# Kernel optimization log

Measured on AMD Instinct MI355X. Metric: run time of the kernel, lower is better.

The kernel has to match this reference:

```python
import jax, jax.numpy as jnp
import numpy as np

N, E, D_IN, D_H, D_OUT, L = 100000, 1000000, 128, 64, 40, 7
MSG_EPS = 1e-7   # GENConv message epsilon
BN_EPS = 1e-5    # torch BatchNorm1d eps
T = 1.0          # softmax temperature (learn_t=False)


def _segment_softmax(logits, seg, n):
    # numerically stable softmax over edges grouped by destination node
    m = jax.ops.segment_max(logits, seg, num_segments=n)
    e = jnp.exp(logits - m[seg])
    s = jax.ops.segment_sum(e, seg, num_segments=n)
    return e / (s[seg] + 1e-16)


def _gen_conv(h, src, dst, W, b):
    # GENConv, aggr='softmax_sg', mlp_layers=1, msg_norm=False
    msg = jax.nn.relu(h[src]) + MSG_EPS                 # [E, D_H]
    w = jax.lax.stop_gradient(_segment_softmax(msg * T, dst, N))
    agg = jax.ops.segment_sum(w * msg, dst, num_segments=N)  # [N, D_H]
    return (h + agg) @ W + b


def _batch_norm(h, gamma, beta):
    mu = jnp.mean(h, axis=0)
    var = jnp.mean(jnp.square(h - mu), axis=0)  # biased var (training mode)
    return gamma * (h - mu) * jax.lax.rsqrt(var + BN_EPS) + beta


def setup_inputs() -> dict:
    key = jax.random.key(0)
    ks = jax.random.split(key, 6)
    x = jax.random.normal(ks[0], (N, D_IN), dtype=jnp.float32)
    edge_index = jax.random.randint(ks[1], (2, E), 0, N, dtype=jnp.int64)
    W_enc = jax.random.normal(ks[2], (D_IN, D_H), dtype=jnp.float32) / np.float32(np.sqrt(D_IN))
    b_enc = jnp.zeros((D_H,), jnp.float32)
    Wg = jax.random.normal(ks[3], (L, D_H, D_H), dtype=jnp.float32) / np.float32(np.sqrt(D_H))
    bg = jnp.zeros((L, D_H), jnp.float32)
    gamma = jnp.ones((L, D_H), jnp.float32)
    beta = jnp.zeros((L, D_H), jnp.float32)
    W_pred = jax.random.normal(ks[4], (D_H, D_OUT), dtype=jnp.float32) / np.float32(np.sqrt(D_H))
    b_pred = jnp.zeros((D_OUT,), jnp.float32)
    return {"x": x, "edge_index": edge_index, "W_enc": W_enc, "b_enc": b_enc,
            "Wg": Wg, "bg": bg, "gamma": gamma, "beta": beta,
            "W_pred": W_pred, "b_pred": b_pred}


def reference(x, edge_index, W_enc, b_enc, Wg, bg, gamma, beta, W_pred, b_pred):
    src, dst = edge_index[0], edge_index[1]
    h = x @ W_enc + b_enc                               # node encoder
    h = _gen_conv(h, src, dst, Wg[0], bg[0])            # first conv (res+)
    for layer in range(1, L):                            # BN->ReLU->Conv->Res
        h2 = jax.nn.relu(_batch_norm(h, gamma[layer - 1], beta[layer - 1]))
        h = _gen_conv(h2, src, dst, Wg[layer], bg[layer]) + h
    h = jax.nn.relu(_batch_norm(h, gamma[L - 1], beta[L - 1]))
    logits = h @ W_pred + b_pred
    return jax.nn.log_softmax(logits, axis=-1)
```

## Files before the change

### kernel.cpp

```cpp
#include <hip/hip_runtime.h>
#include <math.h>

#define NN 100000
#define NE 1000000
#define DH 64
#define DIN 128
#define DOUT 40
#define NL 7
#define SCAN_B 1024
#define NBLK ((NN + SCAN_B - 1) / SCAN_B)
#define NGRP (NN / 16)
#define LBLK ((NGRP + 3) / 4)
#define COLB_CAP (NE + 16 * NN + 64)
#define QS 16.0f
#define IQS 0.0625f

typedef _Float16 v8h __attribute__((ext_vector_type(8)));
typedef float v4f __attribute__((ext_vector_type(4)));

__global__ __launch_bounds__(256) void k_count2(const int* __restrict__ dst,
                                                int* __restrict__ cnt,
                                                int* __restrict__ pi) {
  int i = blockIdx.x * 256 + threadIdx.x;
  if (i < NE) pi[i] = atomicAdd(&cnt[dst[i]], 1);
}

__global__ __launch_bounds__(SCAN_B) void k_scan1(const int* __restrict__ cnt,
                                                  int* __restrict__ rp16,
                                                  int* __restrict__ bsum) {
  __shared__ int buf[SCAN_B];
  int i = blockIdx.x * SCAN_B + threadIdx.x;
  int v = (i < NN) ? ((cnt[i] + 15) & ~15) : 0;
  buf[threadIdx.x] = v;
  __syncthreads();
  for (int off = 1; off < SCAN_B; off <<= 1) {
    int t = (threadIdx.x >= off) ? buf[threadIdx.x - off] : 0;
    __syncthreads();
    buf[threadIdx.x] += t;
    __syncthreads();
  }
  if (i < NN) rp16[i] = buf[threadIdx.x] - v;
  if (threadIdx.x == SCAN_B - 1) bsum[blockIdx.x] = buf[SCAN_B - 1];
}

__global__ __launch_bounds__(128) void k_scan2(int* __restrict__ bsum) {
  __shared__ int buf[128];
  int v = (threadIdx.x < NBLK) ? bsum[threadIdx.x] : 0;
  buf[threadIdx.x] = v;
  __syncthreads();
  for (int off = 1; off < 128; off <<= 1) {
    int t = (threadIdx.x >= off) ? buf[threadIdx.x - off] : 0;
    __syncthreads();
    buf[threadIdx.x] += t;
    __syncthreads();
  }
  if (threadIdx.x < NBLK) bsum[threadIdx.x] = buf[threadIdx.x] - v;
}

__global__ __launch_bounds__(SCAN_B) void k_scan3(int* __restrict__ rp16,
                                                  const int* __restrict__ bsum) {
  int i = blockIdx.x * SCAN_B + threadIdx.x;
  if (i < NN) rp16[i] += bsum[blockIdx.x];
}

__global__ __launch_bounds__(256) void k_place(const int* __restrict__ src,
                                               const int* __restrict__ dst,
                                               const int* __restrict__ rp16,
                                               const int* __restrict__ pi,
                                               int* __restrict__ colb) {
  int i = blockIdx.x * 256 + threadIdx.x;
  if (i < NE) colb[rp16[dst[i]] + pi[i]] = src[i] * DH;
}

__global__ __launch_bounds__(256) void k_enc_mfma(const float* __restrict__ x,
                                                  const float* __restrict__ W,
                                                  const float* __restrict__ b,
                                                  float* __restrict__ h) {
  __shared__ _Float16 Atile[4][2048];
  const int tid = threadIdx.x;
  const int w = tid >> 6, lane = tid & 63;
  const int gid = blockIdx.x * 4 + w;
  if (gid >= NGRP) return;
  const int row = lane & 15, hi = lane >> 4;

  v8h bf[4][4];
#pragma unroll
  for (int kt = 0; kt < 4; ++kt)
#pragma unroll
    for (int ct = 0; ct < 4; ++ct)
#pragma unroll
      for (int j = 0; j < 8; ++j)
        bf[kt][ct][j] = (_Float16)W[(kt * 32 + hi * 8 + j) * DH + ct * 16 + row];

  const int base = gid * 16;
  _Float16* At = &Atile[w][0];
#pragma unroll 4
  for (int i = 0; i < 16; ++i) {
    float v0 = x[(size_t)(base + i) * DIN + lane];
    float v1 = x[(size_t)(base + i) * DIN + 64 + lane];
    int swi = (i & 7) << 4;
    At[(i * 256 + ((lane * 2) ^ swi)) >> 1] = (_Float16)v0;
    At[(i * 256 + 128 + ((lane * 2) ^ swi)) >> 1] = (_Float16)v1;
  }
  const int sw = (row & 7) << 4;
  v8h a[4];
#pragma unroll
  for (int kt = 0; kt < 4; ++kt) {
    int off = (kt & 1) * 64 + hi * 16;
    a[kt] = *(const v8h*)&At[(row * 256 + (kt >> 1) * 128 + (off ^ sw)) >> 1];
  }
  v4f c0 = {0, 0, 0, 0}, c1 = {0, 0, 0, 0}, c2 = {0, 0, 0, 0}, c3 = {0, 0, 0, 0};
#pragma unroll
  for (int kt = 0; kt < 4; ++kt) {
    c0 = __builtin_amdgcn_mfma_f32_16x16x32_f16(a[kt], bf[kt][0], c0, 0, 0, 0);
    c1 = __builtin_amdgcn_mfma_f32_16x16x32_f16(a[kt], bf[kt][1], c1, 0, 0, 0);
    c2 = __builtin_amdgcn_mfma_f32_16x16x32_f16(a[kt], bf[kt][2], c2, 0, 0, 0);
    c3 = __builtin_amdgcn_mfma_f32_16x16x32_f16(a[kt], bf[kt][3], c3, 0, 0, 0);
  }
  float b0 = b[row], b1 = b[16 + row], b2 = b[32 + row], b3 = b[48 + row];
#pragma unroll
  for (int reg = 0; reg < 4; ++reg) {
    size_t o = (size_t)(base + hi * 4 + reg) * DH;
    h[o + row] = c0[reg] + b0;
    h[o + 16 + row] = c1[reg] + b1;
    h[o + 32 + row] = c2[reg] + b2;
    h[o + 48 + row] = c3[reg] + b3;
  }
}

__global__ __launch_bounds__(256) void k_msg(const float* __restrict__ h,
                                             const float* __restrict__ stats_in,
                                             const float* __restrict__ gamma,
                                             const float* __restrict__ beta,
                                             unsigned char* __restrict__ msg) {
  int lane = threadIdx.x & 63;
  float scale = 1.f, shift = 0.f;
  if (stats_in) {
    float mu = stats_in[lane] * (1.0f / NN);
    float var = stats_in[64 + lane] * (1.0f / NN) - mu * mu;
    scale = gamma[lane] * rsqrtf(var + 1e-5f);
    shift = beta[lane] - mu * scale;
  }
  int wid = (blockIdx.x * blockDim.x + threadIdx.x) >> 6;
  int nw = (gridDim.x * blockDim.x) >> 6;
  for (int n = wid; n < NN; n += nw) {
    float r = h[n * DH + lane];
    float v = fmaxf(fmaf(r, scale, shift), 0.f) + 1e-7f;
    msg[n * DH + lane] = (unsigned char)fminf(v * QS + 0.5f, 255.f);
  }
}

__global__ __launch_bounds__(256, 8) void k_agg(const unsigned char* __restrict__ msg,
                                                const int* __restrict__ rp16,
                                                const int* __restrict__ cnt,
                                                const int* __restrict__ colb,
                                                _Float16* __restrict__ agg) {
  const int lane = threadIdx.x & 63;
  const int n = (blockIdx.x * 256 + threadIdx.x) >> 6;
  const int beg = rp16[n];
  const int deg = cnt[n];
  const unsigned char* mb = msg + lane;
  float s = 0.f, t = 0.f;
  for (int j = 0; j < deg; j += 16) {
    int cc[16];
#pragma unroll
    for (int k = 0; k < 16; ++k) cc[k] = colb[beg + j + k];
    float vv[16];
#pragma unroll
    for (int k = 0; k < 16; ++k) vv[k] = (float)mb[cc[k]] * IQS;
    int rem = deg - j;
#pragma unroll
    for (int k = 0; k < 16; ++k) {
      float e = (k < rem) ? __expf(vv[k]) : 0.f;
      s += e;
      t = fmaf(e, vv[k], t);
    }
  }
  agg[(size_t)n * DH + lane] = (_Float16)(t / (s + 1e-16f));
}

__global__ __launch_bounds__(256) void k_mfma(
    const float* __restrict__ h_pre, const _Float16* __restrict__ agg,
    const float* __restrict__ stats_in,
    const float* __restrict__ gamma, const float* __restrict__ beta,
    const float* __restrict__ W, const float* __restrict__ b, int add_res,
    float* __restrict__ hout, float* __restrict__ partial) {
  __shared__ _Float16 Atile[4][1024];
  const int tid = threadIdx.x;
  const int w = tid >> 6, lane = tid & 63;
  const int gid = blockIdx.x * 4 + w;
  const int row = lane & 15, hi = lane >> 4;

  float ss0 = 0, ss1 = 0, ss2 = 0, ss3 = 0;
  float qq0 = 0, qq1 = 0, qq2 = 0, qq3 = 0;

  if (gid < NGRP) {
    float scale = 1.f, shift = 0.f;
    if (stats_in) {
      float mu = stats_in[lane] * (1.0f / NN);
      float var = stats_in[64 + lane] * (1.0f / NN) - mu * mu;
      scale = gamma[lane] * rsqrtf(var + 1e-5f);
      shift = beta[lane] - mu * scale;
    }
    v8h bf[2][4];
#pragma unroll
    for (int kt = 0; kt < 2; ++kt)
#pragma unroll
      for (int ct = 0; ct < 4; ++ct)
#pragma unroll
        for (int j = 0; j < 8; ++j)
          bf[kt][ct][j] = (_Float16)W[(kt * 32 + hi * 8 + j) * DH + ct * 16 + row];

    const int base = gid * 16;
    const float* hl = h_pre + lane;
    const _Float16* agl = agg + lane;
    _Float16* At = &Atile[w][0];

    float rawv[16], agv[16];
#pragma unroll
    for (int i = 0; i < 16; ++i) {
      size_t o = (size_t)(base + i) * DH;
      rawv[i] = hl[o];
      agv[i] = (float)agl[o];
    }
    float res[4][4];
    if (add_res) {
#pragma unroll
      for (int reg = 0; reg < 4; ++reg) {
        size_t o = (size_t)(base + hi * 4 + reg) * DH;
        res[reg][0] = h_pre[o + row];
        res[reg][1] = h_pre[o + 16 + row];
        res[reg][2] = h_pre[o + 32 + row];
        res[reg][3] = h_pre[o + 48 + row];
      }
    }
#pragma unroll
    for (int i = 0; i < 16; ++i) {
      float v = stats_in ? fmaxf(fmaf(rawv[i], scale, shift), 0.f) : rawv[i];
      v += agv[i];
      At[(i * 128 + ((lane * 2) ^ ((i & 7) << 4))) >> 1] = (_Float16)v;
    }
    const int sw = (row & 7) << 4;
    v8h a0 = *(const v8h*)&At[((row * 128) + ((hi * 16) ^ sw)) >> 1];
    v8h a1 = *(const v8h*)&At[((row * 128) + ((64 + hi * 16) ^ sw)) >> 1];
    v4f c0 = {0, 0, 0, 0}, c1 = {0, 0, 0, 0}, c2 = {0, 0, 0, 0}, c3 = {0, 0, 0, 0};
    c0 = __builtin_amdgcn_mfma_f32_16x16x32_f16(a0, bf[0][0], c0, 0, 0, 0);
    c0 = __builtin_amdgcn_mfma_f32_16x16x32_f16(a1, bf[1][0], c0, 0, 0, 0);
    c1 = __builtin_amdgcn_mfma_f32_16x16x32_f16(a0, bf[0][1], c1, 0, 0, 0);
    c1 = __builtin_amdgcn_mfma_f32_16x16x32_f16(a1, bf[1][1], c1, 0, 0, 0);
    c2 = __builtin_amdgcn_mfma_f32_16x16x32_f16(a0, bf[0][2], c2, 0, 0, 0);
    c2 = __builtin_amdgcn_mfma_f32_16x16x32_f16(a1, bf[1][2], c2, 0, 0, 0);
    c3 = __builtin_amdgcn_mfma_f32_16x16x32_f16(a0, bf[0][3], c3, 0, 0, 0);
    c3 = __builtin_amdgcn_mfma_f32_16x16x32_f16(a1, bf[1][3], c3, 0, 0, 0);

    float b0 = b[row], b1 = b[16 + row], b2 = b[32 + row], b3 = b[48 + row];
#pragma unroll
    for (int reg = 0; reg < 4; ++reg) {
      size_t o = (size_t)(base + hi * 4 + reg) * DH;
      float a0v = c0[reg] + b0;
      float a1v = c1[reg] + b1;
      float a2v = c2[reg] + b2;
      float a3v = c3[reg] + b3;
      if (add_res) {
        a0v += res[reg][0];
        a1v += res[reg][1];
        a2v += res[reg][2];
        a3v += res[reg][3];
      }
      hout[o + row] = a0v;
      hout[o + 16 + row] = a1v;
      hout[o + 32 + row] = a2v;
      hout[o + 48 + row] = a3v;
      ss0 += a0v; qq0 = fmaf(a0v, a0v, qq0);
      ss1 += a1v; qq1 = fmaf(a1v, a1v, qq1);
      ss2 += a2v; qq2 = fmaf(a2v, a2v, qq2);
      ss3 += a3v; qq3 = fmaf(a3v, a3v, qq3);
    }
  }

#pragma unroll
  for (int off = 16; off <= 32; off <<= 1) {
    ss0 += __shfl_xor(ss0, off, 64); ss1 += __shfl_xor(ss1, off, 64);
    ss2 += __shfl_xor(ss2, off, 64); ss3 += __shfl_xor(ss3, off, 64);
    qq0 += __shfl_xor(qq0, off, 64); qq1 += __shfl_xor(qq1, off, 64);
    qq2 += __shfl_xor(qq2, off, 64); qq3 += __shfl_xor(qq3, off, 64);
  }
  __syncthreads();
  float* Sr = (float*)&Atile[0][0];
  if (lane < 16) {
    Sr[w * 128 + lane] = ss0;       Sr[w * 128 + 16 + lane] = ss1;
    Sr[w * 128 + 32 + lane] = ss2;  Sr[w * 128 + 48 + lane] = ss3;
    Sr[w * 128 + 64 + lane] = qq0;  Sr[w * 128 + 80 + lane] = qq1;
    Sr[w * 128 + 96 + lane] = qq2;  Sr[w * 128 + 112 + lane] = qq3;
  }
  __syncthreads();
  if (tid < 128) {
    float vsum = Sr[tid] + Sr[128 + tid] + Sr[256 + tid] + Sr[384 + tid];
    partial[(size_t)blockIdx.x * 128 + tid] = vsum;
  }
}

__global__ __launch_bounds__(256) void k_red(const float* __restrict__ partial,
                                             float* __restrict__ stats) {
  const int f = blockIdx.x;
  float acc = 0.f;
  for (int i = threadIdx.x; i < LBLK; i += 256)
    acc += partial[(size_t)i * 128 + f];
  __shared__ float buf[256];
  buf[threadIdx.x] = acc;
  __syncthreads();
  for (int off = 128; off >= 1; off >>= 1) {
    if (threadIdx.x < off) buf[threadIdx.x] += buf[threadIdx.x + off];
    __syncthreads();
  }
  if (threadIdx.x == 0) stats[f] = buf[0];
}

__global__ __launch_bounds__(256) void k_pred_mfma(
    const float* __restrict__ h_pre, const float* __restrict__ stats_in,
    const float* __restrict__ gamma, const float* __restrict__ beta,
    const float* __restrict__ Wp, const float* __restrict__ bp,
    float* __restrict__ out) {
  __shared__ _Float16 Atile[4][1024];
  const int tid = threadIdx.x;
  const int w = tid >> 6, lane = tid & 63;
  const int gid = blockIdx.x * 4 + w;
  if (gid >= NGRP) return;
  const int row = lane & 15, hi = lane >> 4;

  float mu = stats_in[lane] * (1.0f / NN);
  float var = stats_in[64 + lane] * (1.0f / NN) - mu * mu;
  float scale = gamma[lane] * rsqrtf(var + 1e-5f);
  float shift = beta[lane] - mu * scale;

  v8h bf[2][3];
#pragma unroll
  for (int kt = 0; kt < 2; ++kt)
#pragma unroll
    for (int ct = 0; ct < 3; ++ct) {
      int n = ct * 16 + row;
#pragma unroll
      for (int j = 0; j < 8; ++j)
        bf[kt][ct][j] =
            (n < DOUT) ? (_Float16)Wp[(kt * 32 + hi * 8 + j) * DOUT + n]
                       : (_Float16)0.f;
    }

  const int base = gid * 16;
  const float* hl = h_pre + lane;
  _Float16* At = &Atile[w][0];
#pragma unroll 4
  for (int i = 0; i < 16; ++i) {
    float raw = hl[(size_t)(base + i) * DH];
    float v = fmaxf(fmaf(raw, scale, shift), 0.f);
    At[(i * 128 + ((lane * 2) ^ ((i & 7) << 4))) >> 1] = (_Float16)v;
  }
  const int sw = (row & 7) << 4;
  v8h a0 = *(const v8h*)&At[((row * 128) + ((hi * 16) ^ sw)) >> 1];
  v8h a1 = *(const v8h*)&At[((row * 128) + ((64 + hi * 16) ^ sw)) >> 1];
  v4f c0 = {0, 0, 0, 0}, c1 = {0, 0, 0, 0}, c2 = {0, 0, 0, 0};
  c0 = __builtin_amdgcn_mfma_f32_16x16x32_f16(a0, bf[0][0], c0, 0, 0, 0);
  c0 = __builtin_amdgcn_mfma_f32_16x16x32_f16(a1, bf[1][0], c0, 0, 0, 0);
  c1 = __builtin_amdgcn_mfma_f32_16x16x32_f16(a0, bf[0][1], c1, 0, 0, 0);
  c1 = __builtin_amdgcn_mfma_f32_16x16x32_f16(a1, bf[1][1], c1, 0, 0, 0);
  c2 = __builtin_amdgcn_mfma_f32_16x16x32_f16(a0, bf[0][2], c2, 0, 0, 0);
  c2 = __builtin_amdgcn_mfma_f32_16x16x32_f16(a1, bf[1][2], c2, 0, 0, 0);

  float bp0 = bp[row], bp1 = bp[16 + row];
  float bp2 = (32 + row < DOUT) ? bp[32 + row] : 0.f;
  bool v2 = (32 + row) < DOUT;
#pragma unroll
  for (int reg = 0; reg < 4; ++reg) {
    float l0 = c0[reg] + bp0;
    float l1 = c1[reg] + bp1;
    float l2 = v2 ? (c2[reg] + bp2) : -INFINITY;
    float xm = fmaxf(fmaxf(l0, l1), l2);
#pragma unroll
    for (int off = 1; off <= 8; off <<= 1) xm = fmaxf(xm, __shfl_xor(xm, off, 64));
    float e = __expf(l0 - xm) + __expf(l1 - xm) + (v2 ? __expf(l2 - xm) : 0.f);
#pragma unroll
    for (int off = 1; off <= 8; off <<= 1) e += __shfl_xor(e, off, 64);
    float ls = xm + __logf(e);
    size_t o = (size_t)(base + hi * 4 + reg) * DOUT;
    out[o + row] = l0 - ls;
    out[o + 16 + row] = l1 - ls;
    if (v2) out[o + 32 + row] = l2 - ls;
  }
}

extern "C" void kernel_launch(void* const* d_in, const int* in_sizes, int n_in,
                              void* d_out, int out_size, void* d_ws, size_t ws_size,
                              hipStream_t stream) {
  const float* x      = (const float*)d_in[0];
  const int*   ei     = (const int*)d_in[1];
  const float* W_enc  = (const float*)d_in[2];
  const float* b_enc  = (const float*)d_in[3];
  const float* Wg     = (const float*)d_in[4];
  const float* bg     = (const float*)d_in[5];
  const float* gamma  = (const float*)d_in[6];
  const float* beta   = (const float*)d_in[7];
  const float* W_pred = (const float*)d_in[8];
  const float* b_pred = (const float*)d_in[9];
  float* out = (float*)d_out;

  const int* src = ei;
  const int* dst = ei + NE;

  char* p = (char*)d_ws;
  auto alloc = [&](size_t bytes) -> void* {
    void* r = (void*)p;
    p += (bytes + 255) & ~(size_t)255;
    return r;
  };
  float*         hA      = (float*)alloc((size_t)NN * DH * 4);
  float*         hB      = (float*)alloc((size_t)NN * DH * 4);
  unsigned char* msg     = (unsigned char*)alloc((size_t)NN * DH);
  _Float16*      agg     = (_Float16*)alloc((size_t)NN * DH * 2);
  int*           rp16    = (int*)alloc((size_t)(NN + 1) * 4);
  int*           pi      = (int*)alloc((size_t)NE * 4);
  int*           cnt     = (int*)alloc((size_t)NN * 4);
  int*           colb    = (int*)alloc((size_t)COLB_CAP * 4);
  int*           bsum    = (int*)alloc((size_t)NBLK * 4);
  float*         stats   = (float*)alloc((size_t)NL * 128 * 4);
  float*         partial = (float*)alloc((size_t)LBLK * 128 * 4);

  hipMemsetAsync(cnt, 0, (size_t)NN * 4, stream);
  hipMemsetAsync(colb, 0, (size_t)COLB_CAP * 4, stream);

  k_count2<<<(NE + 255) / 256, 256, 0, stream>>>(dst, cnt, pi);
  k_scan1<<<NBLK, SCAN_B, 0, stream>>>(cnt, rp16, bsum);
  k_scan2<<<1, 128, 0, stream>>>(bsum);
  k_scan3<<<NBLK, SCAN_B, 0, stream>>>(rp16, bsum);
  k_place<<<(NE + 255) / 256, 256, 0, stream>>>(src, dst, rp16, pi, colb);

  k_enc_mfma<<<LBLK, 256, 0, stream>>>(x, W_enc, b_enc, hA);

  const int MSG_BLOCKS = 1024;
  const int AGG_BLOCKS = NN * 64 / 256;

  k_msg<<<MSG_BLOCKS, 256, 0, stream>>>(hA, nullptr, nullptr, nullptr, msg);
  k_agg<<<AGG_BLOCKS, 256, 0, stream>>>(msg, rp16, cnt, colb, agg);
  k_mfma<<<LBLK, 256, 0, stream>>>(
      hA, agg, nullptr, nullptr, nullptr, Wg, bg, 0, hB, partial);
  k_red<<<128, 256, 0, stream>>>(partial, stats);

  float* h = hB;
  float* hn = hA;
  for (int l = 1; l < NL; ++l) {
    const float* st = stats + (size_t)(l - 1) * 128;
    const float* g  = gamma + (size_t)(l - 1) * DH;
    const float* be = beta + (size_t)(l - 1) * DH;
    k_msg<<<MSG_BLOCKS, 256, 0, stream>>>(h, st, g, be, msg);
    k_agg<<<AGG_BLOCKS, 256, 0, stream>>>(msg, rp16, cnt, colb, agg);
    k_mfma<<<LBLK, 256, 0, stream>>>(
        h, agg, st, g, be,
        Wg + (size_t)l * DH * DH, bg + (size_t)l * DH, 1,
        hn, partial);
    k_red<<<128, 256, 0, stream>>>(partial, stats + (size_t)l * 128);
    float* tmp = h; h = hn; hn = tmp;
  }

  k_pred_mfma<<<LBLK, 256, 0, stream>>>(
      h, stats + (size_t)(NL - 1) * 128,
      gamma + (size_t)(NL - 1) * DH, beta + (size_t)(NL - 1) * DH,
      W_pred, b_pred, out);
}
```

Measured before the change: 554.0 us.

## Pad CSR to 8 with a zero-message sentinel row and split count atomics

Degree padding in the CSR drops from 16 to 8. Padded slots now point at a zeroed sentinel message row (offset DH), so the aggregation loop runs without per-element masking and afterwards subtracts the padding's exp(0) contributions from the denominator. Edge counting spreads atomics over four sub-counters per node to reduce contention, which needs extra per-node sub-offsets in the scan and placement kernels. Row begin and degree are made wave-uniform with readfirstlane. The cost is extra scan work and memory, and more exp calls on padded slots.

Measured after the change: 517.5 us. -6.6%, faster.

```diff
diff --git a/kernel.cpp b/kernel.cpp
--- a/kernel.cpp
+++ b/kernel.cpp
@@ -11,27 +11,37 @@
 #define NBLK ((NN + SCAN_B - 1) / SCAN_B)
 #define NGRP (NN / 16)
 #define LBLK ((NGRP + 3) / 4)
-#define COLB_CAP (NE + 16 * NN + 64)
+#define COLB_CAP (NE + 8 * NN + 64)
 #define QS 16.0f
 #define IQS 0.0625f
 
 typedef _Float16 v8h __attribute__((ext_vector_type(8)));
 typedef float v4f __attribute__((ext_vector_type(4)));
 
-__global__ __launch_bounds__(256) void k_count2(const int* __restrict__ dst,
-                                                int* __restrict__ cnt,
+__global__ __launch_bounds__(256) void k_count4(const int* __restrict__ dst,
+                                                int* __restrict__ cnt4,
                                                 int* __restrict__ pi) {
   int i = blockIdx.x * 256 + threadIdx.x;
-  if (i < NE) pi[i] = atomicAdd(&cnt[dst[i]], 1);
-}
-
-__global__ __launch_bounds__(SCAN_B) void k_scan1(const int* __restrict__ cnt,
-                                                  int* __restrict__ rp16,
+  if (i < NE) pi[i] = atomicAdd(&cnt4[(size_t)(i & 3) * NN + dst[i]], 1);
+}
+
+__global__ __launch_bounds__(SCAN_B) void k_scan1(const int* __restrict__ cnt4,
+                                                  int* __restrict__ cnt,
+                                                  int* __restrict__ rp8,
+                                                  int* __restrict__ rp8s,
                                                   int* __restrict__ bsum) {
   __shared__ int buf[SCAN_B];
   int i = blockIdx.x * SCAN_B + threadIdx.x;
-  int v = (i < NN) ? ((cnt[i] + 15) & ~15) : 0;
-  buf[threadIdx.x] = v;
+  int c0 = 0, c1 = 0, c2 = 0, c3 = 0;
+  if (i < NN) {
+    c0 = cnt4[i];
+    c1 = cnt4[(size_t)NN + i];
+    c2 = cnt4[(size_t)2 * NN + i];
+    c3 = cnt4[(size_t)3 * NN + i];
+  }
+  int tot = c0 + c1 + c2 + c3;
+  int t8 = (tot + 7) & ~7;
+  buf[threadIdx.x] = t8;
   __syncthreads();
   for (int off = 1; off < SCAN_B; off <<= 1) {
     int t = (threadIdx.x >= off) ? buf[threadIdx.x - off] : 0;
@@ -39,7 +49,15 @@
     buf[threadIdx.x] += t;
     __syncthreads();
   }
-  if (i < NN) rp16[i] = buf[threadIdx.x] - v;
+  if (i < NN) {
+    int excl = buf[threadIdx.x] - t8;
+    cnt[i] = tot;
+    rp8[i] = excl;
+    rp8s[4 * i] = excl;
+    rp8s[4 * i + 1] = excl + c0;
+    rp8s[4 * i + 2] = excl + c0 + c1;
+    rp8s[4 * i + 3] = excl + c0 + c1 + c2;
+  }
   if (threadIdx.x == SCAN_B - 1) bsum[blockIdx.x] = buf[SCAN_B - 1];
 }
 
@@ -57,19 +75,28 @@
   if (threadIdx.x < NBLK) bsum[threadIdx.x] = buf[threadIdx.x] - v;
 }
 
-__global__ __launch_bounds__(SCAN_B) void k_scan3(int* __restrict__ rp16,
+__global__ __launch_bounds__(SCAN_B) void k_scan3(int* __restrict__ rp8,
+                                                  int* __restrict__ rp8s,
                                                   const int* __restrict__ bsum) {
   int i = blockIdx.x * SCAN_B + threadIdx.x;
-  if (i < NN) rp16[i] += bsum[blockIdx.x];
+  if (i < NN) {
+    int b = bsum[blockIdx.x];
+    rp8[i] += b;
+    rp8s[4 * i] += b;
+    rp8s[4 * i + 1] += b;
+    rp8s[4 * i + 2] += b;
+    rp8s[4 * i + 3] += b;
+  }
 }
 
 __global__ __launch_bounds__(256) void k_place(const int* __restrict__ src,
                                                const int* __restrict__ dst,
-                                               const int* __restrict__ rp16,
+                                               const int* __restrict__ rp8s,
                                                const int* __restrict__ pi,
                                                int* __restrict__ colb) {
   int i = blockIdx.x * 256 + threadIdx.x;
-  if (i < NE) colb[rp16[dst[i]] + pi[i]] = src[i] * DH;
+  if (i < NE)
+    colb[rp8s[4 * dst[i] + (i & 3)] + pi[i]] = src[i] * DH + DH;
 }
 
 __global__ __launch_bounds__(256) void k_enc_mfma(const float* __restrict__ x,
@@ -146,36 +173,37 @@
   for (int n = wid; n < NN; n += nw) {
     float r = h[n * DH + lane];
     float v = fmaxf(fmaf(r, scale, shift), 0.f) + 1e-7f;
-    msg[n * DH + lane] = (unsigned char)fminf(v * QS + 0.5f, 255.f);
+    msg[DH + n * DH + lane] = (unsigned char)fminf(v * QS + 0.5f, 255.f);
   }
 }
 
 __global__ __launch_bounds__(256, 8) void k_agg(const unsigned char* __restrict__ msg,
-                                                const int* __restrict__ rp16,
+                                                const int* __restrict__ rp8,
                                                 const int* __restrict__ cnt,
                                                 const int* __restrict__ colb,
                                                 _Float16* __restrict__ agg) {
   const int lane = threadIdx.x & 63;
   const int n = (blockIdx.x * 256 + threadIdx.x) >> 6;
-  const int beg = rp16[n];
-  const int deg = cnt[n];
+  const int beg = __builtin_amdgcn_readfirstlane(rp8[n]);
+  const int deg = __builtin_amdgcn_readfirstlane(cnt[n]);
+  const int pdeg = (deg + 7) & ~7;
   const unsigned char* mb = msg + lane;
   float s = 0.f, t = 0.f;
-  for (int j = 0; j < deg; j += 16) {
-    int cc[16];
-#pragma unroll
-    for (int k = 0; k < 16; ++k) cc[k] = colb[beg + j + k];
-    float vv[16];
-#pragma unroll
-    for (int k = 0; k < 16; ++k) vv[k] = (float)mb[cc[k]] * IQS;
-    int rem = deg - j;
-#pragma unroll
-    for (int k = 0; k < 16; ++k) {
-      float e = (k < rem) ? __expf(vv[k]) : 0.f;
+  for (int j = 0; j < pdeg; j += 8) {
+    int cc[8];
+#pragma unroll
+    for (int k = 0; k < 8; ++k) cc[k] = colb[beg + j + k];
+    float vv[8];
+#pragma unroll
+    for (int k = 0; k < 8; ++k) vv[k] = (float)mb[cc[k]] * IQS;
+#pragma unroll
+    for (int k = 0; k < 8; ++k) {
+      float e = __expf(vv[k]);
       s += e;
       t = fmaf(e, vv[k], t);
     }
   }
+  s -= (float)(pdeg - deg);
   agg[(size_t)n * DH + lane] = (_Float16)(t / (s + 1e-16f));
 }
 
@@ -414,24 +442,27 @@
   };
   float*         hA      = (float*)alloc((size_t)NN * DH * 4);
   float*         hB      = (float*)alloc((size_t)NN * DH * 4);
-  unsigned char* msg     = (unsigned char*)alloc((size_t)NN * DH);
+  unsigned char* msg     = (unsigned char*)alloc((size_t)(NN + 1) * DH);
   _Float16*      agg     = (_Float16*)alloc((size_t)NN * DH * 2);
-  int*           rp16    = (int*)alloc((size_t)(NN + 1) * 4);
+  int*           rp8     = (int*)alloc((size_t)NN * 4);
+  int*           rp8s    = (int*)alloc((size_t)NN * 4 * 4);
   int*           pi      = (int*)alloc((size_t)NE * 4);
   int*           cnt     = (int*)alloc((size_t)NN * 4);
+  int*           cnt4    = (int*)alloc((size_t)NN * 4 * 4);
   int*           colb    = (int*)alloc((size_t)COLB_CAP * 4);
   int*           bsum    = (int*)alloc((size_t)NBLK * 4);
   float*         stats   = (float*)alloc((size_t)NL * 128 * 4);
   float*         partial = (float*)alloc((size_t)LBLK * 128 * 4);
 
-  hipMemsetAsync(cnt, 0, (size_t)NN * 4, stream);
+  hipMemsetAsync(cnt4, 0, (size_t)NN * 16, stream);
   hipMemsetAsync(colb, 0, (size_t)COLB_CAP * 4, stream);
-
-  k_count2<<<(NE + 255) / 256, 256, 0, stream>>>(dst, cnt, pi);
-  k_scan1<<<NBLK, SCAN_B, 0, stream>>>(cnt, rp16, bsum);
+  hipMemsetAsync(msg, 0, DH, stream);
+
+  k_count4<<<(NE + 255) / 256, 256, 0, stream>>>(dst, cnt4, pi);
+  k_scan1<<<NBLK, SCAN_B, 0, stream>>>(cnt4, cnt, rp8, rp8s, bsum);
   k_scan2<<<1, 128, 0, stream>>>(bsum);
-  k_scan3<<<NBLK, SCAN_B, 0, stream>>>(rp16, bsum);
-  k_place<<<(NE + 255) / 256, 256, 0, stream>>>(src, dst, rp16, pi, colb);
+  k_scan3<<<NBLK, SCAN_B, 0, stream>>>(rp8, rp8s, bsum);
+  k_place<<<(NE + 255) / 256, 256, 0, stream>>>(src, dst, rp8s, pi, colb);
 
   k_enc_mfma<<<LBLK, 256, 0, stream>>>(x, W_enc, b_enc, hA);
 
@@ -439,7 +470,7 @@
   const int AGG_BLOCKS = NN * 64 / 256;
 
   k_msg<<<MSG_BLOCKS, 256, 0, stream>>>(hA, nullptr, nullptr, nullptr, msg);
-  k_agg<<<AGG_BLOCKS, 256, 0, stream>>>(msg, rp16, cnt, colb, agg);
+  k_agg<<<AGG_BLOCKS, 256, 0, stream>>>(msg, rp8, cnt, colb, agg);
   k_mfma<<<LBLK, 256, 0, stream>>>(
       hA, agg, nullptr, nullptr, nullptr, Wg, bg, 0, hB, partial);
   k_red<<<128, 256, 0, stream>>>(partial, stats);
@@ -451,7 +482,7 @@
     const float* g  = gamma + (size_t)(l - 1) * DH;
     const float* be = beta + (size_t)(l - 1) * DH;
     k_msg<<<MSG_BLOCKS, 256, 0, stream>>>(h, st, g, be, msg);
-    k_agg<<<AGG_BLOCKS, 256, 0, stream>>>(msg, rp16, cnt, colb, agg);
+    k_agg<<<AGG_BLOCKS, 256, 0, stream>>>(msg, rp8, cnt, colb, agg);
     k_mfma<<<LBLK, 256, 0, stream>>>(
         h, agg, st, g, be,
         Wg + (size_t)l * DH * DH, bg + (size_t)l * DH, 1,
```
